# Performance work log

Hardware: AMD Instinct MI355X
Metric: run time of the kernel (lower is better)

## Reference

```python
import jax, jax.numpy as jnp
import numpy as np

B, T = 64, 256
E = 300          # embedding_size
H = 512          # hidden_num
L = 9            # label_size
V = 30000        # vocab_size
S = 30000        # sentence_size


def setup_inputs() -> dict:
    key = jax.random.key(0)
    ks = jax.random.split(key, 14)
    D = 2 * E
    inp = {
        "text": jax.random.randint(ks[0], (B, T), 0, V, dtype=jnp.int32),
        "sentence": jax.random.randint(ks[1], (B, T), 0, S, dtype=jnp.int32),
        "labels": jax.random.randint(ks[2], (B, T), 0, L, dtype=jnp.int32),
        "word_emb": jax.random.normal(ks[3], (V, E), jnp.float32) * 0.05,
        "sent_emb": jax.random.normal(ks[4], (S, E), jnp.float32) * 0.05,
        "Wk_f": jax.random.normal(ks[5], (D, 4 * H), jnp.float32) / np.sqrt(D).astype(np.float32),
        "Wr_f": jax.random.normal(ks[6], (H, 4 * H), jnp.float32) / np.sqrt(H).astype(np.float32),
        "b_f": jnp.zeros((4 * H,), jnp.float32),
        "Wk_b": jax.random.normal(ks[7], (D, 4 * H), jnp.float32) / np.sqrt(D).astype(np.float32),
        "Wr_b": jax.random.normal(ks[8], (H, 4 * H), jnp.float32) / np.sqrt(H).astype(np.float32),
        "b_b": jnp.zeros((4 * H,), jnp.float32),
        "Wd": jax.random.normal(ks[9], (2 * H, L), jnp.float32) / np.sqrt(2 * H).astype(np.float32),
        "bd": jnp.zeros((L,), jnp.float32),
        "trans": jax.random.uniform(ks[10], (L, L), jnp.float32),
    }
    return inp


def lstm(x, Wk, Wr, b):
    # x: [B,T,D]; Keras LSTM gate order i,f,g,o; sigmoid recurrent act, tanh act.
    xz = jnp.einsum('btd,dk->btk', x, Wk) + b  # one big GEMM for all timesteps
    h0 = jnp.zeros((x.shape[0], Wr.shape[0]), x.dtype)

    def step(carry, z_t):
        h, c = carry
        z = z_t + h @ Wr
        i, f, g, o = jnp.split(z, 4, axis=-1)
        c = jax.nn.sigmoid(f) * c + jax.nn.sigmoid(i) * jnp.tanh(g)
        h = jax.nn.sigmoid(o) * jnp.tanh(c)
        return (h, c), h

    _, hs = jax.lax.scan(step, (h0, h0), jnp.swapaxes(xz, 0, 1))
    return jnp.swapaxes(hs, 0, 1)  # [B,T,H]


def crf_log_likelihood(logits, labels, mask, trans):
    maskf = mask.astype(logits.dtype)
    # unary score of the gold path
    unary = jnp.take_along_axis(logits, labels[..., None], axis=-1)[..., 0]  # [B,T]
    unary = jnp.sum(unary * maskf, axis=-1)
    # binary (transition) score
    binary = trans[labels[:, :-1], labels[:, 1:]]  # [B,T-1]
    binary = jnp.sum(binary * maskf[:, 1:], axis=-1)
    # forward algorithm (log partition), masked steps carry alpha
    logits_tm = jnp.swapaxes(logits, 0, 1)  # [T,B,L]
    mask_tm = jnp.swapaxes(mask, 0, 1)

    def step(alpha, inputs):
        logit_t, m_t = inputs
        new = jax.nn.logsumexp(alpha[:, :, None] + trans[None], axis=1) + logit_t
        return jnp.where(m_t[:, None], new, alpha), None

    alpha, _ = jax.lax.scan(step, logits_tm[0], (logits_tm[1:], mask_tm[1:]))
    log_norm = jax.nn.logsumexp(alpha, axis=-1)
    return unary + binary - log_norm


def crf_decode(logits, trans, mask):
    b, t, l = logits.shape
    logits_tm = jnp.swapaxes(logits, 0, 1)
    mask_tm = jnp.swapaxes(mask, 0, 1)
    ident = jnp.broadcast_to(jnp.arange(l)[None], (b, l))

    def step(alpha, inputs):
        logit_t, m_t = inputs
        score = alpha[:, :, None] + trans[None]      # [B,L,L]
        bp = jnp.argmax(score, axis=1)               # [B,L]
        new = jnp.max(score, axis=1) + logit_t
        alpha = jnp.where(m_t[:, None], new, alpha)
        bp = jnp.where(m_t[:, None], bp, ident)      # identity through padding
        return alpha, bp

    alpha, bps = jax.lax.scan(step, logits_tm[0], (logits_tm[1:], mask_tm[1:]))
    last = jnp.argmax(alpha, axis=-1)  # [B]

    def back(tag, bp):
        prev = jnp.take_along_axis(bp, tag[:, None], axis=1)[:, 0]
        return prev, prev

    _, tags = jax.lax.scan(back, last, bps, reverse=True)  # [T-1,B], original time order
    tags = jnp.concatenate([tags, last[None]], axis=0)     # [T,B]
    return jnp.swapaxes(tags, 0, 1).astype(jnp.int32)


def reference(text, sentence, labels, word_emb, sent_emb, Wk_f, Wr_f, b_f,
              Wk_b, Wr_b, b_b, Wd, bd, trans):
    x = jnp.concatenate([word_emb[text], sent_emb[sentence]], axis=-1)  # [B,T,2E]
    hf = lstm(x, Wk_f, Wr_f, b_f)
    hb = lstm(x[:, ::-1], Wk_b, Wr_b, b_b)[:, ::-1]
    h = jnp.concatenate([hf, hb], axis=-1)  # [B,T,2H]
    logits = h @ Wd + bd                    # [B,T,L]
    text_lens = jnp.sum((text != 0).astype(jnp.int32), axis=-1)
    mask = jnp.arange(T)[None, :] < text_lens[:, None]
    log_likelihood = crf_log_likelihood(logits, labels, mask, trans)
    pred_tags = crf_decode(logits, trans, mask)
    return logits, text_lens, log_likelihood, pred_tags
```

## Files before the change

### kernel.cpp

```cpp
#include <hip/hip_runtime.h>
#include <hip/hip_bf16.h>
#include <math.h>

#define BB 64
#define TT 256
#define EE 300
#define DD 600
#define KP 608
#define HH 512
#define G4 2048
#define LL 9
#define NT (BB*TT)

typedef __attribute__((ext_vector_type(8))) short short8;
typedef __attribute__((ext_vector_type(4))) float floatx4;

#define XZF_OFF  ((size_t)0)
#define XZ_BYTES ((size_t)NT * G4 * 2)
#define XZB_OFF  (XZF_OFF + XZ_BYTES)
#define HSR_OFF  (XZB_OFF + XZ_BYTES)
#define HS_BYTES ((size_t)NT * HH * 2)
#define HSF_OFF  (HSR_OFF)
#define HSB_OFF  (HSR_OFF + HS_BYTES)
#define XG_OFF   (HSR_OFF)
#define WKT_OFF  (HSR_OFF + 19922944)
#define WRT_OFF  (HSR_OFF + (size_t)2 * HS_BYTES)
#define BK_OFF   (WRT_OFF + 4194304)
#define FAST_OFF (BK_OFF + 524288)
#define EX_BYTES ((size_t)2 * 2 * BB * HH * 4)
#define FLAGS_OFF (FAST_OFF + 524288)
#define WDT_OFF  XZF_OFF

#define OUT_LOGITS 0
#define OUT_LENS   (BB*TT*LL)
#define OUT_LL     (OUT_LENS + BB)
#define OUT_TAGS   (OUT_LL + BB)

__global__ __launch_bounds__(256) void prep_xg(
    const int* __restrict__ text, const int* __restrict__ sent,
    const float* __restrict__ wemb, const float* __restrict__ semb,
    __hip_bfloat16* __restrict__ xg)
{
    int n = blockIdx.x;
    int ti = text[n], si = sent[n];
    __hip_bfloat16* o = xg + (size_t)n * KP;
    for (int k = threadIdx.x; k < KP; k += 256) {
        float v = 0.f;
        if (k < EE)      v = wemb[(size_t)ti * EE + k];
        else if (k < DD) v = semb[(size_t)si * EE + (k - EE)];
        o[k] = __float2bfloat16(v);
    }
}

__global__ __launch_bounds__(256) void transpose_w(
    const float* __restrict__ Wf, const float* __restrict__ Wb,
    __hip_bfloat16* __restrict__ outT, int Din, int Dpad)
{
    int dir = blockIdx.z;
    const float* W = dir ? Wb : Wf;
    __hip_bfloat16* o = outT + (size_t)dir * G4 * Dpad;
    int n0 = blockIdx.x * 64, d0 = blockIdx.y * 64;
    __shared__ float tile[64][65];
    int c = threadIdx.x & 63, r4 = threadIdx.x >> 6;
    #pragma unroll
    for (int rr = 0; rr < 64; rr += 4) {
        int d = d0 + rr + r4;
        tile[rr + r4][c] = (d < Din) ? W[(size_t)d * G4 + n0 + c] : 0.f;
    }
    __syncthreads();
    #pragma unroll
    for (int rr = 0; rr < 64; rr += 4) {
        int n = n0 + rr + r4;
        int d = d0 + c;
        if (d < Dpad) o[(size_t)n * Dpad + d] = __float2bfloat16(tile[c][rr + r4]);
    }
}

__global__ __launch_bounds__(256) void prep_wdT(
    const float* __restrict__ Wd, __hip_bfloat16* __restrict__ WdT)
{
    for (int i = threadIdx.x + blockIdx.x * 256; i < 16 * 1024; i += gridDim.x * 256) {
        int nn = i >> 10, k = i & 1023;
        WdT[i] = __float2bfloat16(nn < LL ? Wd[(size_t)k * LL + nn] : 0.f);
    }
}

__global__ __launch_bounds__(256) void embed_gemm(
    const __hip_bfloat16* __restrict__ xg,
    const __hip_bfloat16* __restrict__ WkT,
    const float* __restrict__ b_f, const float* __restrict__ b_b,
    __hip_bfloat16* __restrict__ xz_f, __hip_bfloat16* __restrict__ xz_b)
{
    int dir = blockIdx.z;
    const __hip_bfloat16* wt = WkT + (size_t)dir * G4 * KP;
    const float* bias = dir ? b_b : b_f;
    __hip_bfloat16* xz = dir ? xz_b : xz_f;

    int n0 = blockIdx.x * 128;
    int c0 = blockIdx.y * 64;
    int wave = threadIdx.x >> 6, lane = threadIdx.x & 63;
    int m0 = (wave & 1) * 64;
    int nn0 = (wave >> 1) * 32;
    int lm = lane & 15, lk8 = (lane >> 4) * 8;

    const short8 *ap[4], *bp2[2];
    #pragma unroll
    for (int i = 0; i < 4; ++i)
        ap[i] = (const short8*)(xg + (size_t)(n0 + m0 + i*16 + lm) * KP + lk8);
    #pragma unroll
    for (int i = 0; i < 2; ++i)
        bp2[i] = (const short8*)(wt + (size_t)(c0 + nn0 + i*16 + lm) * KP + lk8);

    floatx4 acc[4][2] = {};
    for (int kc = 0; kc < KP/32; ++kc) {
        short8 a0 = ap[0][kc*4], a1 = ap[1][kc*4], a2 = ap[2][kc*4], a3 = ap[3][kc*4];
        short8 b0 = bp2[0][kc*4], b1 = bp2[1][kc*4];
        acc[0][0] = __builtin_amdgcn_mfma_f32_16x16x32_bf16(a0, b0, acc[0][0], 0,0,0);
        acc[0][1] = __builtin_amdgcn_mfma_f32_16x16x32_bf16(a0, b1, acc[0][1], 0,0,0);
        acc[1][0] = __builtin_amdgcn_mfma_f32_16x16x32_bf16(a1, b0, acc[1][0], 0,0,0);
        acc[1][1] = __builtin_amdgcn_mfma_f32_16x16x32_bf16(a1, b1, acc[1][1], 0,0,0);
        acc[2][0] = __builtin_amdgcn_mfma_f32_16x16x32_bf16(a2, b0, acc[2][0], 0,0,0);
        acc[2][1] = __builtin_amdgcn_mfma_f32_16x16x32_bf16(a2, b1, acc[2][1], 0,0,0);
        acc[3][0] = __builtin_amdgcn_mfma_f32_16x16x32_bf16(a3, b0, acc[3][0], 0,0,0);
        acc[3][1] = __builtin_amdgcn_mfma_f32_16x16x32_bf16(a3, b1, acc[3][1], 0,0,0);
    }

    int lr = (lane >> 4) * 4;
    #pragma unroll
    for (int ni = 0; ni < 2; ++ni) {
        int col = c0 + nn0 + ni*16 + lm;
        float bs = bias[col];
        #pragma unroll
        for (int mi = 0; mi < 4; ++mi) {
            #pragma unroll
            for (int r = 0; r < 4; ++r) {
                int row = n0 + m0 + mi*16 + lr + r;
                xz[(size_t)row * G4 + col] = __float2bfloat16(acc[mi][ni][r] + bs);
            }
        }
    }
}

__device__ __forceinline__ void load16_sc0(const unsigned long long* base,
                                           int tid, unsigned long long* v)
{
    #pragma unroll
    for (int q = 0; q < 16; ++q) {
        const unsigned long long* ap = base + tid + 256 * q;
        asm volatile("global_load_dwordx2 %0, %1, off sc0"
                     : "=v"(v[q]) : "v"(ap));
    }
    asm volatile("s_waitcnt vmcnt(0)" ::: "memory");
}

__device__ __forceinline__ void store_sc0(unsigned long long* p,
                                          unsigned long long val)
{
    asm volatile("global_store_dwordx2 %0, %1, off sc0"
                 :: "v"(p), "v"(val) : "memory");
}

__device__ __forceinline__ unsigned load_u32_sc0(const unsigned* p)
{
    unsigned r;
    asm volatile("global_load_dword %0, %1, off sc0\n\ts_waitcnt vmcnt(0)"
                 : "=v"(r) : "v"(p) : "memory");
    return r;
}

__device__ __forceinline__ void store_u32_sc0(unsigned* p, unsigned v)
{
    asm volatile("global_store_dword %0, %1, off sc0" :: "v"(p), "v"(v) : "memory");
}

__global__ __launch_bounds__(256, 1) void lstm_coop(
    const __hip_bfloat16* __restrict__ xz_f, const __hip_bfloat16* __restrict__ xz_b,
    const __hip_bfloat16* __restrict__ WrT,
    unsigned* __restrict__ bk,
    unsigned* __restrict__ fast,
    unsigned* __restrict__ flags,
    __hip_bfloat16* __restrict__ hs_f, __hip_bfloat16* __restrict__ hs_b)
{
    int blk = blockIdx.x;
    int g = blk & 7;
    int member = blk >> 3;
    int dir = g >> 2;
    int r0 = (g & 3) * 16;
    int h0 = member * 16;
    int tid = threadIdx.x;
    int gate = tid >> 6, lane = tid & 63;
    int lm = lane & 15, lk8 = (lane >> 4) * 8;

    const __hip_bfloat16* xz = dir ? xz_b : xz_f;
    __hip_bfloat16* hs = dir ? hs_b : hs_f;
    const __hip_bfloat16* wrt = WrT + (size_t)dir * G4 * HH;
    unsigned* bkd = bk + (size_t)dir * 2 * BB * HH;
    unsigned* fsd = fast + (size_t)dir * 2 * BB * HH;
    const unsigned* gfl = flags + (g << 5);
    unsigned* myflag = flags + (g << 5) + member;

    short8 bfrag[16];
    {
        const short8* wp = (const short8*)(wrt + (size_t)(gate*HH + h0 + lm) * HH + lk8);
        #pragma unroll
        for (int kc = 0; kc < 16; ++kc) bfrag[kc] = wp[kc*4];
    }

    __shared__ unsigned short htile[16][520];
    __shared__ float zbuf[4][16][17];

    int er = tid >> 3, ec = (tid & 7) * 2;
    float c0st = 0.f, c1st = 0.f;
    int zr = (lane >> 4) * 4;

    bool fastok = true;
    int fallcnt = 0;

    for (int t = 0; t < TT; ++t) {
        int tok = dir ? (TT - 1 - t) : t;
        size_t soff = (size_t)(t & 1) * BB * HH + (size_t)r0 * HH;
        const unsigned long long pat =
            ((unsigned long long)(unsigned)t << 48) |
            ((unsigned long long)(unsigned)t << 16);

        float xzv[4];
        #pragma unroll
        for (int r = 0; r < 4; ++r) {
            int n = (r0 + zr + r) * TT + tok;
            xzv[r] = __bfloat162float(xz[(size_t)n * G4 + gate*HH + h0 + lm]);
        }

        unsigned long long v[16];
        bool ok = false;
        if (fastok) {
            const unsigned long long* fsrc = (const unsigned long long*)(fsd + soff);
            load16_sc0(fsrc, tid, v);
            unsigned long long bad = 0;
            #pragma unroll
            for (int q = 0; q < 16; ++q)
                bad |= (v[q] ^ pat) & 0xFFFF0000FFFF0000ULL;
            if (__all(bad == 0)) {
                ok = true;
            } else {
                unsigned need = (unsigned)t;
                bool flagok = false;
                for (int spin = 0; spin < 96; ++spin) {
                    unsigned f = load_u32_sc0(gfl + (lane & 31));
                    if (__all(f >= need)) { flagok = true; break; }
                    __builtin_amdgcn_s_sleep(2);
                }
                if (flagok) {
                    load16_sc0(fsrc, tid, v);
                    bad = 0;
                    #pragma unroll
                    for (int q = 0; q < 16; ++q)
                        bad |= (v[q] ^ pat) & 0xFFFF0000FFFF0000ULL;
                    if (__all(bad == 0)) ok = true;
                }
                if (!ok) { if (++fallcnt >= 3) fastok = false; }
            }
        }
        if (!ok) {
            const unsigned long long* bsrc = (const unsigned long long*)(bkd + soff);
            for (;;) {
                #pragma unroll
                for (int q = 0; q < 16; ++q)
                    v[q] = __hip_atomic_load(bsrc + tid + 256*q,
                            __ATOMIC_RELAXED, __HIP_MEMORY_SCOPE_AGENT);
                unsigned long long bad = 0;
                #pragma unroll
                for (int q = 0; q < 16; ++q)
                    bad |= (v[q] ^ pat) & 0xFFFF0000FFFF0000ULL;
                if (bad == 0) break;
                __builtin_amdgcn_s_sleep(2);
            }
        }

        #pragma unroll
        for (int q = 0; q < 16; ++q) {
            unsigned lo = (unsigned)(v[q] & 0xffffu);
            unsigned hi = (unsigned)((v[q] >> 32) & 0xffffu);
            *(unsigned*)&htile[q][tid * 2] = lo | (hi << 16);
        }
        __syncthreads();

        floatx4 acc = {};
        #pragma unroll
        for (int kc = 0; kc < 16; ++kc) {
            short8 a = *(const short8*)&htile[lm][kc * 32 + lk8];
            acc = __builtin_amdgcn_mfma_f32_16x16x32_bf16(a, bfrag[kc], acc, 0,0,0);
        }

        #pragma unroll
        for (int r = 0; r < 4; ++r)
            zbuf[gate][zr + r][lm] = acc[r] + xzv[r];
        __syncthreads();

        if (tid < 128) {
            float zi0 = zbuf[0][er][ec],   zi1 = zbuf[0][er][ec+1];
            float zf0 = zbuf[1][er][ec],   zf1 = zbuf[1][er][ec+1];
            float zg0 = zbuf[2][er][ec],   zg1 = zbuf[2][er][ec+1];
            float zo0 = zbuf[3][er][ec],   zo1 = zbuf[3][er][ec+1];
            float si0 = 1.f/(1.f+__expf(-zi0)), si1 = 1.f/(1.f+__expf(-zi1));
            float sf0 = 1.f/(1.f+__expf(-zf0)), sf1 = 1.f/(1.f+__expf(-zf1));
            float so0 = 1.f/(1.f+__expf(-zo0)), so1 = 1.f/(1.f+__expf(-zo1));
            c0st = sf0 * c0st + si0 * tanhf(zg0);
            c1st = sf1 * c1st + si1 * tanhf(zg1);
            float h0v = so0 * tanhf(c0st);
            float h1v = so1 * tanhf(c1st);
            unsigned u0 = (unsigned)__builtin_bit_cast(unsigned short, __float2bfloat16(h0v));
            unsigned u1 = (unsigned)__builtin_bit_cast(unsigned short, __float2bfloat16(h1v));
            unsigned tg = (unsigned)(t + 1) << 16;
            unsigned long long pay =
                ((unsigned long long)(tg | u1) << 32) | (unsigned long long)(tg | u0);
            size_t eoff = (size_t)((t+1) & 1) * BB * HH + (size_t)(r0 + er) * HH + h0 + ec;
            store_sc0((unsigned long long*)(fsd + eoff), pay);
            __hip_atomic_store((unsigned long long*)(bkd + eoff), pay,
                               __ATOMIC_RELAXED, __HIP_MEMORY_SCOPE_AGENT);
            *(unsigned*)(hs + ((size_t)(r0 + er) * TT + tok) * HH + h0 + ec) =
                u0 | (u1 << 16);
        }
        __syncthreads();
        if (tid == 0)
            store_u32_sc0(myflag, (unsigned)(t + 1));
    }
}

__global__ __launch_bounds__(256) void logits_kernel(
    const __hip_bfloat16* __restrict__ hs_f, const __hip_bfloat16* __restrict__ hs_b,
    const __hip_bfloat16* __restrict__ WdT, const float* __restrict__ bd,
    float* __restrict__ out)
{
    int n0 = blockIdx.x * 64;
    int wave = threadIdx.x >> 6, lane = threadIdx.x & 63;
    int lm = lane & 15, lk8 = (lane >> 4) * 8;
    int nw = n0 + wave * 16;
    const short8* af = (const short8*)(hs_f + (size_t)(nw + lm) * HH + lk8);
    const short8* ab = (const short8*)(hs_b + (size_t)(nw + lm) * HH + lk8);
    const short8* bw = (const short8*)(WdT + (size_t)lm * 1024 + lk8);
    floatx4 acc = {};
    #pragma unroll
    for (int kc = 0; kc < 16; ++kc) {
        acc = __builtin_amdgcn_mfma_f32_16x16x32_bf16(af[kc*4], bw[kc*4], acc, 0,0,0);
        acc = __builtin_amdgcn_mfma_f32_16x16x32_bf16(ab[kc*4], bw[(kc+16)*4], acc, 0,0,0);
    }
    if (lm < LL) {
        float bv = bd[lm];
        #pragma unroll
        for (int r = 0; r < 4; ++r) {
            int n = nw + (lane >> 4) * 4 + r;
            out[(size_t)n * LL + lm] = acc[r] + bv;
        }
    }
}

__global__ __launch_bounds__(256) void crf_kernel(
    const float* __restrict__ logits, const int* __restrict__ text,
    const int* __restrict__ labels, const float* __restrict__ trans,
    float* __restrict__ out_lens, float* __restrict__ out_ll,
    float* __restrict__ out_tags)
{
    int b = blockIdx.x, tid = threadIdx.x;
    const float* lg = logits + (size_t)b * TT * LL;
    const int* lab = labels + b * TT;

    __shared__ float lgs[TT * LL];
    __shared__ float trs[81];
    __shared__ unsigned char bps[255 * LL + 1];
    __shared__ float partial[256];
    __shared__ int ired[256];
    __shared__ float tagf[TT];

    for (int i = tid; i < TT * LL; i += 256) lgs[i] = lg[i];
    if (tid < 81) trs[tid] = trans[tid];
    ired[tid] = (text[b * TT + tid] != 0) ? 1 : 0;
    __syncthreads();
    for (int s = 128; s > 0; s >>= 1) {
        if (tid < s) ired[tid] += ired[tid + s];
        __syncthreads();
    }
    int len = ired[0];
    if (tid == 0) out_lens[b] = (float)len;

    float up = 0.f;
    for (int t = tid; t < TT; t += 256) {
        float m = (t < len) ? 1.f : 0.f;
        up += m * lgs[t * LL + lab[t]];
        if (t >= 1) up += m * trs[lab[t - 1] * LL + lab[t]];
    }
    partial[tid] = up;
    __syncthreads();
    for (int s = 128; s > 0; s >>= 1) {
        if (tid < s) partial[tid] += partial[tid + s];
        __syncthreads();
    }

    if (tid < 64) {
        int lane = tid;
        int j = (lane < LL) ? lane : 0;
        float trj[LL];
        #pragma unroll
        for (int i = 0; i < LL; ++i) trj[i] = trs[i * LL + j];
        float alpha = lgs[j];
        float vit = alpha;
        for (int t = 1; t < TT; ++t) {
            bool m = t < len;
            float lgv = lgs[t * LL + j];
            float ta[LL];
            float mx = -1e30f, bv = -1e30f; int bi = 0;
            #pragma unroll
            for (int i = 0; i < LL; ++i) {
                float av = __shfl(alpha, i);
                float vv = __shfl(vit, i);
                ta[i] = av + trj[i];
                mx = fmaxf(mx, ta[i]);
                float sv = vv + trj[i];
                if (sv > bv) { bv = sv; bi = i; }
            }
            float s = 0.f;
            #pragma unroll
            for (int i = 0; i < LL; ++i) s += __expf(ta[i] - mx);
            float newa = mx + __logf(s) + lgv;
            float newv = bv + lgv;
            if (m) { alpha = newa; vit = newv; }
            if (lane < LL) bps[(t - 1) * LL + lane] = (unsigned char)(m ? bi : lane);
        }
        float aX[LL], vX[LL];
        #pragma unroll
        for (int i = 0; i < LL; ++i) { aX[i] = __shfl(alpha, i); vX[i] = __shfl(vit, i); }
        if (lane == 0) {
            float mx = -1e30f;
            #pragma unroll
            for (int i = 0; i < LL; ++i) mx = fmaxf(mx, aX[i]);
            float s = 0.f;
            #pragma unroll
            for (int i = 0; i < LL; ++i) s += __expf(aX[i] - mx);
            out_ll[b] = partial[0] - (mx + __logf(s));

            float bvv = vX[0]; int last = 0;
            #pragma unroll
            for (int i = 1; i < LL; ++i) if (vX[i] > bvv) { bvv = vX[i]; last = i; }
            tagf[TT - 1] = (float)last;
            int tg = last;
            for (int s2 = TT - 2; s2 >= 0; --s2) {
                tg = bps[s2 * LL + tg];
                tagf[s2] = (float)tg;
            }
        }
    }
    __syncthreads();
    out_tags[b * TT + tid] = tagf[tid];
}

extern "C" void kernel_launch(void* const* d_in, const int* in_sizes, int n_in,
                              void* d_out, int out_size, void* d_ws, size_t ws_size,
                              hipStream_t stream)
{
    const int*   text  = (const int*)d_in[0];
    const int*   sent  = (const int*)d_in[1];
    const int*   labels= (const int*)d_in[2];
    const float* wemb  = (const float*)d_in[3];
    const float* semb  = (const float*)d_in[4];
    const float* Wk_f  = (const float*)d_in[5];
    const float* Wr_f  = (const float*)d_in[6];
    const float* b_f   = (const float*)d_in[7];
    const float* Wk_b  = (const float*)d_in[8];
    const float* Wr_b  = (const float*)d_in[9];
    const float* b_b   = (const float*)d_in[10];
    const float* Wd    = (const float*)d_in[11];
    const float* bd    = (const float*)d_in[12];
    const float* trans = (const float*)d_in[13];
    float* out = (float*)d_out;

    char* ws = (char*)d_ws;
    __hip_bfloat16* xz_f = (__hip_bfloat16*)(ws + XZF_OFF);
    __hip_bfloat16* xz_b = (__hip_bfloat16*)(ws + XZB_OFF);
    __hip_bfloat16* hs_f = (__hip_bfloat16*)(ws + HSF_OFF);
    __hip_bfloat16* hs_b = (__hip_bfloat16*)(ws + HSB_OFF);
    __hip_bfloat16* xg   = (__hip_bfloat16*)(ws + XG_OFF);
    __hip_bfloat16* WkT  = (__hip_bfloat16*)(ws + WKT_OFF);
    __hip_bfloat16* WrT  = (__hip_bfloat16*)(ws + WRT_OFF);
    unsigned*       bk   = (unsigned*)(ws + BK_OFF);
    unsigned*       fast = (unsigned*)(ws + FAST_OFF);
    unsigned*       flg  = (unsigned*)(ws + FLAGS_OFF);
    __hip_bfloat16* WdT  = (__hip_bfloat16*)(ws + WDT_OFF);

    prep_xg <<<NT,  256, 0, stream>>>(text, sent, wemb, semb, xg);
    transpose_w<<<dim3(G4/64, (KP+63)/64, 2), 256, 0, stream>>>(Wk_f, Wk_b, WkT, DD, KP);
    transpose_w<<<dim3(G4/64, HH/64, 2),      256, 0, stream>>>(Wr_f, Wr_b, WrT, HH, HH);
    hipMemsetAsync(ws + BK_OFF, 0, 2 * EX_BYTES + 1024, stream);

    embed_gemm<<<dim3(NT/128, G4/64, 2), 256, 0, stream>>>(
        xg, WkT, b_f, b_b, xz_f, xz_b);

    {
        void* args[] = { (void*)&xz_f, (void*)&xz_b, (void*)&WrT,
                         (void*)&bk, (void*)&fast, (void*)&flg,
                         (void*)&hs_f, (void*)&hs_b };
        hipLaunchCooperativeKernel((const void*)lstm_coop, dim3(256), dim3(256),
                                   args, 0, stream);
    }

    prep_wdT<<<16, 256, 0, stream>>>(Wd, WdT);
    logits_kernel<<<NT/64, 256, 0, stream>>>(hs_f, hs_b, WdT, bd, out + OUT_LOGITS);
    crf_kernel<<<BB, 256, 0, stream>>>(out + OUT_LOGITS, text, labels, trans,
                                       out + OUT_LENS, out + OUT_LL, out + OUT_TAGS);
}
```

Baseline: 1.429 ms.

## Widen LSTM recurrence blocks to 64 hidden units and prefetch next-step xz

The cooperative LSTM kernel now runs 64 blocks instead of 256, and each block handles 64 hidden columns using four MFMA tiles per gate with four times the register-resident Wr fragments. This cuts the number of blocks taking part in each group's per-step cross-block handshake from 32 to 8. The xz inputs for the next timestep are prefetched into registers during the current step. Stores of h are widened to dwordx4, and some barriers are replaced by raw s_barrier. In exchange, each block does more serial MFMA and activation work per step, register pressure rises sharply, and fewer CUs are used.

```diff
diff --git a/kernel.cpp b/kernel.cpp
--- a/kernel.cpp
+++ b/kernel.cpp
@@ -14,6 +14,7 @@
 
 typedef __attribute__((ext_vector_type(8))) short short8;
 typedef __attribute__((ext_vector_type(4))) float floatx4;
+typedef __attribute__((ext_vector_type(4))) unsigned uintx4;
 
 #define XZF_OFF  ((size_t)0)
 #define XZ_BYTES ((size_t)NT * G4 * 2)
@@ -153,10 +154,11 @@
     asm volatile("s_waitcnt vmcnt(0)" ::: "memory");
 }
 
-__device__ __forceinline__ void store_sc0(unsigned long long* p,
-                                          unsigned long long val)
-{
-    asm volatile("global_store_dwordx2 %0, %1, off sc0"
+__device__ __forceinline__ void store16_sc0(unsigned* p, unsigned a, unsigned b,
+                                            unsigned c, unsigned d)
+{
+    uintx4 val = {a, b, c, d};
+    asm volatile("global_store_dwordx4 %0, %1, off sc0"
                  :: "v"(p), "v"(val) : "memory");
 }
 
@@ -171,6 +173,15 @@
 __device__ __forceinline__ void store_u32_sc0(unsigned* p, unsigned v)
 {
     asm volatile("global_store_dword %0, %1, off sc0" :: "v"(p), "v"(v) : "memory");
+}
+
+__device__ __forceinline__ void block_barrier_raw()
+{
+    asm volatile("" ::: "memory");
+    __builtin_amdgcn_sched_barrier(0);
+    __builtin_amdgcn_s_barrier();
+    __builtin_amdgcn_sched_barrier(0);
+    asm volatile("" ::: "memory");
 }
 
 __global__ __launch_bounds__(256, 1) void lstm_coop(
@@ -186,10 +197,11 @@
     int member = blk >> 3;
     int dir = g >> 2;
     int r0 = (g & 3) * 16;
-    int h0 = member * 16;
+    int h0 = member * 64;
     int tid = threadIdx.x;
     int gate = tid >> 6, lane = tid & 63;
     int lm = lane & 15, lk8 = (lane >> 4) * 8;
+    int zr = (lane >> 4) * 4;
 
     const __hip_bfloat16* xz = dir ? xz_b : xz_f;
     __hip_bfloat16* hs = dir ? hs_b : hs_f;
@@ -199,19 +211,34 @@
     const unsigned* gfl = flags + (g << 5);
     unsigned* myflag = flags + (g << 5) + member;
 
-    short8 bfrag[16];
+    short8 bfrag[16][4];
+    #pragma unroll
+    for (int ni = 0; ni < 4; ++ni) {
+        const short8* wp = (const short8*)(wrt +
+            (size_t)(gate*HH + h0 + ni*16 + lm) * HH + lk8);
+        #pragma unroll
+        for (int kc = 0; kc < 16; ++kc) bfrag[kc][ni] = wp[kc*4];
+    }
+
+    __shared__ unsigned short htile[16][520];
+    __shared__ float zbuf[4][16][67];
+
+    int erow = tid >> 4;
+    int ec0  = (tid & 15) * 4;
+    float cst[4] = {0.f, 0.f, 0.f, 0.f};
+
+    unsigned short xz_cur[16], xz_nxt[16];
     {
-        const short8* wp = (const short8*)(wrt + (size_t)(gate*HH + h0 + lm) * HH + lk8);
-        #pragma unroll
-        for (int kc = 0; kc < 16; ++kc) bfrag[kc] = wp[kc*4];
-    }
-
-    __shared__ unsigned short htile[16][520];
-    __shared__ float zbuf[4][16][17];
-
-    int er = tid >> 3, ec = (tid & 7) * 2;
-    float c0st = 0.f, c1st = 0.f;
-    int zr = (lane >> 4) * 4;
+        int tok0 = dir ? (TT - 1) : 0;
+        #pragma unroll
+        for (int r = 0; r < 4; ++r) {
+            const __hip_bfloat16* p = xz +
+                ((size_t)((r0 + zr + r) * TT + tok0)) * G4 + gate*HH + h0 + lm;
+            #pragma unroll
+            for (int ni = 0; ni < 4; ++ni)
+                xz_cur[ni*4 + r] = *(const unsigned short*)(p + ni*16);
+        }
+    }
 
     bool fastok = true;
     int fallcnt = 0;
@@ -222,13 +249,6 @@
         const unsigned long long pat =
             ((unsigned long long)(unsigned)t << 48) |
             ((unsigned long long)(unsigned)t << 16);
-
-        float xzv[4];
-        #pragma unroll
-        for (int r = 0; r < 4; ++r) {
-            int n = (r0 + zr + r) * TT + tok;
-            xzv[r] = __bfloat162float(xz[(size_t)n * G4 + gate*HH + h0 + lm]);
-        }
 
         unsigned long long v[16];
         bool ok = false;
@@ -245,7 +265,7 @@
                 unsigned need = (unsigned)t;
                 bool flagok = false;
                 for (int spin = 0; spin < 96; ++spin) {
-                    unsigned f = load_u32_sc0(gfl + (lane & 31));
+                    unsigned f = load_u32_sc0(gfl + (lane & 7));
                     if (__all(f >= need)) { flagok = true; break; }
                     __builtin_amdgcn_s_sleep(2);
                 }
@@ -284,45 +304,82 @@
         }
         __syncthreads();
 
-        floatx4 acc = {};
+        if (t + 1 < TT) {
+            int tokn = dir ? (TT - 2 - t) : (t + 1);
+            #pragma unroll
+            for (int r = 0; r < 4; ++r) {
+                const __hip_bfloat16* p = xz +
+                    ((size_t)((r0 + zr + r) * TT + tokn)) * G4 + gate*HH + h0 + lm;
+                #pragma unroll
+                for (int ni = 0; ni < 4; ++ni)
+                    xz_nxt[ni*4 + r] = *(const unsigned short*)(p + ni*16);
+            }
+        }
+
+        floatx4 acc[4] = {};
         #pragma unroll
         for (int kc = 0; kc < 16; ++kc) {
-            short8 a = *(const short8*)&htile[lm][kc * 32 + lk8];
-            acc = __builtin_amdgcn_mfma_f32_16x16x32_bf16(a, bfrag[kc], acc, 0,0,0);
-        }
-
-        #pragma unroll
-        for (int r = 0; r < 4; ++r)
-            zbuf[gate][zr + r][lm] = acc[r] + xzv[r];
-        __syncthreads();
-
-        if (tid < 128) {
-            float zi0 = zbuf[0][er][ec],   zi1 = zbuf[0][er][ec+1];
-            float zf0 = zbuf[1][er][ec],   zf1 = zbuf[1][er][ec+1];
-            float zg0 = zbuf[2][er][ec],   zg1 = zbuf[2][er][ec+1];
-            float zo0 = zbuf[3][er][ec],   zo1 = zbuf[3][er][ec+1];
-            float si0 = 1.f/(1.f+__expf(-zi0)), si1 = 1.f/(1.f+__expf(-zi1));
-            float sf0 = 1.f/(1.f+__expf(-zf0)), sf1 = 1.f/(1.f+__expf(-zf1));
-            float so0 = 1.f/(1.f+__expf(-zo0)), so1 = 1.f/(1.f+__expf(-zo1));
-            c0st = sf0 * c0st + si0 * tanhf(zg0);
-            c1st = sf1 * c1st + si1 * tanhf(zg1);
-            float h0v = so0 * tanhf(c0st);
-            float h1v = so1 * tanhf(c1st);
-            unsigned u0 = (unsigned)__builtin_bit_cast(unsigned short, __float2bfloat16(h0v));
-            unsigned u1 = (unsigned)__builtin_bit_cast(unsigned short, __float2bfloat16(h1v));
-            unsigned tg = (unsigned)(t + 1) << 16;
-            unsigned long long pay =
-                ((unsigned long long)(tg | u1) << 32) | (unsigned long long)(tg | u0);
-            size_t eoff = (size_t)((t+1) & 1) * BB * HH + (size_t)(r0 + er) * HH + h0 + ec;
-            store_sc0((unsigned long long*)(fsd + eoff), pay);
-            __hip_atomic_store((unsigned long long*)(bkd + eoff), pay,
-                               __ATOMIC_RELAXED, __HIP_MEMORY_SCOPE_AGENT);
-            *(unsigned*)(hs + ((size_t)(r0 + er) * TT + tok) * HH + h0 + ec) =
-                u0 | (u1 << 16);
-        }
-        __syncthreads();
+            short8 a = *(const short8*)&htile[lm][kc*32 + lk8];
+            #pragma unroll
+            for (int ni = 0; ni < 4; ++ni)
+                acc[ni] = __builtin_amdgcn_mfma_f32_16x16x32_bf16(
+                              a, bfrag[kc][ni], acc[ni], 0,0,0);
+        }
+
+        #pragma unroll
+        for (int ni = 0; ni < 4; ++ni) {
+            #pragma unroll
+            for (int r = 0; r < 4; ++r) {
+                float xv = __bfloat162float(
+                    __builtin_bit_cast(__hip_bfloat16, xz_cur[ni*4 + r]));
+                zbuf[gate][zr + r][ni*16 + lm] = acc[ni][r] + xv;
+            }
+        }
+
+        asm volatile("s_waitcnt lgkmcnt(0)" ::: "memory");
+        block_barrier_raw();
+
+        float h4[4];
+        #pragma unroll
+        for (int j = 0; j < 4; ++j) {
+            float zi = zbuf[0][erow][ec0 + j];
+            float zf = zbuf[1][erow][ec0 + j];
+            float zg = zbuf[2][erow][ec0 + j];
+            float zo = zbuf[3][erow][ec0 + j];
+            float si = 1.f/(1.f+__expf(-zi));
+            float sf = 1.f/(1.f+__expf(-zf));
+            float so = 1.f/(1.f+__expf(-zo));
+            cst[j] = sf * cst[j] + si * tanhf(zg);
+            h4[j] = so * tanhf(cst[j]);
+        }
+        unsigned tg = (unsigned)(t + 1) << 16;
+        unsigned u0 = tg | (unsigned)__builtin_bit_cast(unsigned short, __float2bfloat16(h4[0]));
+        unsigned u1 = tg | (unsigned)__builtin_bit_cast(unsigned short, __float2bfloat16(h4[1]));
+        unsigned u2 = tg | (unsigned)__builtin_bit_cast(unsigned short, __float2bfloat16(h4[2]));
+        unsigned u3 = tg | (unsigned)__builtin_bit_cast(unsigned short, __float2bfloat16(h4[3]));
+
+        size_t eoff = (size_t)((t+1) & 1) * BB * HH + (size_t)(r0 + erow) * HH + h0 + ec0;
+        store16_sc0(fsd + eoff, u0, u1, u2, u3);
+        asm volatile("s_waitcnt vmcnt(0)" ::: "memory");
+        unsigned long long p01 = ((unsigned long long)u1 << 32) | u0;
+        unsigned long long p23 = ((unsigned long long)u3 << 32) | u2;
+        __hip_atomic_store((unsigned long long*)(bkd + eoff), p01,
+                           __ATOMIC_RELAXED, __HIP_MEMORY_SCOPE_AGENT);
+        __hip_atomic_store((unsigned long long*)(bkd + eoff) + 1, p23,
+                           __ATOMIC_RELAXED, __HIP_MEMORY_SCOPE_AGENT);
+        unsigned long long hp =
+            ((unsigned long long)(u3 & 0xffffu) << 48) |
+            ((unsigned long long)(u2 & 0xffffu) << 32) |
+            ((unsigned long long)(u1 & 0xffffu) << 16) |
+            (unsigned long long)(u0 & 0xffffu);
+        *(unsigned long long*)(hs + ((size_t)(r0 + erow) * TT + tok) * HH + h0 + ec0) = hp;
+
+        block_barrier_raw();
         if (tid == 0)
             store_u32_sc0(myflag, (unsigned)(t + 1));
+
+        #pragma unroll
+        for (int i = 0; i < 16; ++i) xz_cur[i] = xz_nxt[i];
     }
 }
 
@@ -497,7 +554,7 @@
         void* args[] = { (void*)&xz_f, (void*)&xz_b, (void*)&WrT,
                          (void*)&bk, (void*)&fast, (void*)&flg,
                          (void*)&hs_f, (void*)&hs_b };
-        hipLaunchCooperativeKernel((const void*)lstm_coop, dim3(256), dim3(256),
+        hipLaunchCooperativeKernel((const void*)lstm_coop, dim3(64), dim3(256),
                                    args, 0, stream);
     }
 
```

Measured after the change: 1.735 ms. 1.21x slower.
